# Optimization experiments

Hardware: AMD Instinct MI355X
Metric: run time of the kernel (lower is better)

Reference implementation:

```python
import jax, jax.numpy as jnp
import numpy as np

B, S, D, E, K = 4, 2048, 1024, 8, 2
H = 4 * D  # FFN hidden per expert


def setup_inputs() -> dict:
    key = jax.random.key(0)
    ks = jax.random.split(key, 5)
    s = 0.02  # init scale
    return {
        "x": jax.random.normal(ks[0], (B, S, D), dtype=jnp.float32),
        "Wg": jax.random.normal(ks[1], (D, E), dtype=jnp.float32) * s,
        "bg": jnp.zeros((E,), dtype=jnp.float32),
        "W1": jax.random.normal(ks[2], (E, D, H), dtype=jnp.float32) * s,
        "b1": jnp.zeros((E, H), dtype=jnp.float32),
        "W2": jax.random.normal(ks[3], (E, H, D), dtype=jnp.float32) * s,
        "b2": jnp.zeros((E, D), dtype=jnp.float32),
    }


def reference(x, Wg, bg, W1, b1, W2, b2):
    # Router: softmax over expert logits, then top-k (torch.topk semantics)
    probs = jax.nn.softmax(x @ Wg + bg, axis=-1)      # [B,S,E]
    w, idx = jax.lax.top_k(probs, K)                   # [B,S,K] each
    # Dense all-experts MLP (matches original: every expert runs on every token)
    h = jax.nn.gelu(jnp.einsum('bsd,edh->bseh', x, W1) + b1, approximate=False)  # [B,S,E,H]
    y = jnp.einsum('bseh,ehd->bsed', h, W2) + b2       # [B,S,E,D]
    # One-hot mask + weighted sum == gather selected experts, scale by w, sum over k
    yk = jnp.take_along_axis(y, idx[..., None], axis=2)  # [B,S,K,D]
    return jnp.sum(yk * w[..., None], axis=2)            # [B,S,D]
```

## Files before the change

kernel.cpp:

```cpp
#include <hip/hip_runtime.h>
#include <hip/hip_bf16.h>
#include <math.h>


#define TOK     8192
#define DMODEL  1024
#define NEXP    8
#define HFF     4096
#define NASSIGN 16384
#define SLOTPAD 16512
#define BM      128
#define BN      128
#define BK      64
#define MAXRT   135

typedef __attribute__((ext_vector_type(8))) short s16x8;
typedef __attribute__((ext_vector_type(4))) float f32x4;

__device__ __forceinline__ void gll16(const void* g, void* l) {
  __builtin_amdgcn_global_load_lds((const __attribute__((address_space(1))) void*)g,
                                   (__attribute__((address_space(3))) void*)l, 16, 0, 0);
}

__global__ void transpose_cvt(const float* __restrict__ in, __hip_bfloat16* __restrict__ out,
                              int R, int C) {
  __shared__ float t[64][65];
  const float* src = in + (size_t)blockIdx.z * R * C;
  __hip_bfloat16* dst = out + (size_t)blockIdx.z * R * C;
  const int r0 = blockIdx.y * 64, c0 = blockIdx.x * 64;
  const int tc = threadIdx.x & 63, tr = threadIdx.x >> 6;
#pragma unroll
  for (int i = 0; i < 16; ++i) {
    int r = i * 4 + tr;
    t[r][tc] = src[(size_t)(r0 + r) * C + c0 + tc];
  }
  __syncthreads();
  const int jl = (threadIdx.x & 15) * 4;
  const int cw = threadIdx.x >> 4;
#pragma unroll
  for (int p = 0; p < 4; ++p) {
    const int cc = p * 16 + cw;
    union { ushort4 u; __hip_bfloat16 h[4]; } o;
#pragma unroll
    for (int u = 0; u < 4; ++u) o.h[u] = __float2bfloat16(t[jl + u][cc]);
    *(ushort4*)(dst + (size_t)(c0 + cc) * R + r0 + jl) = o.u;
  }
}

__global__ void router_kernel(const float* __restrict__ x, const float* __restrict__ Wg,
                              const float* __restrict__ bg, int* __restrict__ idx,
                              float* __restrict__ wtok, int* __restrict__ counts) {
  __shared__ int scnt[NEXP];
  if (threadIdx.x < NEXP) scnt[threadIdx.x] = 0;
  __syncthreads();
  const int wave = threadIdx.x >> 6, lane = threadIdx.x & 63;
  const int t = blockIdx.x * 4 + wave;
  float acc[NEXP];
#pragma unroll
  for (int e = 0; e < NEXP; ++e) acc[e] = 0.f;
  const float* xr = x + (size_t)t * DMODEL + lane * 16;
#pragma unroll
  for (int j = 0; j < 4; ++j) {
    float4 xv = *(const float4*)(xr + j * 4);
    const float* wr = Wg + (size_t)(lane * 16 + j * 4) * NEXP;
#pragma unroll
    for (int u = 0; u < 4; ++u) {
      float xs = (&xv.x)[u];
      float4 w0 = *(const float4*)(wr + u * NEXP);
      float4 w1 = *(const float4*)(wr + u * NEXP + 4);
      acc[0] += xs * w0.x; acc[1] += xs * w0.y; acc[2] += xs * w0.z; acc[3] += xs * w0.w;
      acc[4] += xs * w1.x; acc[5] += xs * w1.y; acc[6] += xs * w1.z; acc[7] += xs * w1.w;
    }
  }
#pragma unroll
  for (int off = 32; off >= 1; off >>= 1) {
#pragma unroll
    for (int e = 0; e < NEXP; ++e) acc[e] += __shfl_xor(acc[e], off, 64);
  }
  if (lane == 0) {
    float l[NEXP], m = -1e30f;
#pragma unroll
    for (int e = 0; e < NEXP; ++e) { l[e] = acc[e] + bg[e]; m = fmaxf(m, l[e]); }
    float p[NEXP], s = 0.f;
#pragma unroll
    for (int e = 0; e < NEXP; ++e) { p[e] = expf(l[e] - m); s += p[e]; }
    float inv = 1.f / s;
#pragma unroll
    for (int e = 0; e < NEXP; ++e) p[e] *= inv;
    int i0 = 0; float v0 = p[0];
#pragma unroll
    for (int e = 1; e < NEXP; ++e) if (p[e] > v0) { v0 = p[e]; i0 = e; }
    int i1 = -1; float v1 = -1e30f;
#pragma unroll
    for (int e = 0; e < NEXP; ++e) if (e != i0 && p[e] > v1) { v1 = p[e]; i1 = e; }
    idx[2 * t] = i0; idx[2 * t + 1] = i1;
    wtok[2 * t] = v0; wtok[2 * t + 1] = v1;
    atomicAdd(&scnt[i0], 1); atomicAdd(&scnt[i1], 1);
  }
  __syncthreads();
  if (threadIdx.x < NEXP) atomicAdd(&counts[threadIdx.x], scnt[threadIdx.x]);
}

__global__ void scan_kernel(int* ctrl) {
  if (threadIdx.x == 0 && blockIdx.x == 0) {
    int* counts = ctrl;
    int* cursor = ctrl + 8;
    int* expOff = ctrl + 16;
    int* tro = ctrl + 26;
    expOff[0] = 0; tro[0] = 0;
    for (int e = 0; e < NEXP; ++e) {
      expOff[e + 1] = expOff[e] + counts[e];
      tro[e + 1] = tro[e] + (counts[e] + BM - 1) / BM;
      cursor[e] = expOff[e];
    }
  }
}

__global__ void scatter_kernel(const int* __restrict__ idx, const float* __restrict__ wtok,
                               int* ctrl, int* __restrict__ perm, float* __restrict__ wslot) {
  __shared__ int lcnt[NEXP];
  __shared__ int lbase[NEXP];
  const int t = blockIdx.x * 256 + threadIdx.x;
  if (threadIdx.x < NEXP) lcnt[threadIdx.x] = 0;
  __syncthreads();
  const int e0 = idx[2 * t], e1 = idx[2 * t + 1];
  const int l0 = atomicAdd(&lcnt[e0], 1);
  const int l1 = atomicAdd(&lcnt[e1], 1);
  __syncthreads();
  if (threadIdx.x < NEXP)
    lbase[threadIdx.x] = atomicAdd(&ctrl[8 + threadIdx.x], lcnt[threadIdx.x]);
  __syncthreads();
  const int s0 = lbase[e0] + l0, s1 = lbase[e1] + l1;
  perm[s0] = t; perm[s1] = t;
  wslot[s0] = wtok[2 * t]; wslot[s1] = wtok[2 * t + 1];
}

__global__ void gather_cvt_x(const float* __restrict__ x, const int* __restrict__ perm,
                             __hip_bfloat16* __restrict__ xg) {
  const int slot = blockIdx.x;
  const int t = perm[slot];
  const float4 v = *(const float4*)(x + (size_t)t * DMODEL + threadIdx.x * 4);
  union { ushort4 u; __hip_bfloat16 h[4]; } o;
  o.h[0] = __float2bfloat16(v.x); o.h[1] = __float2bfloat16(v.y);
  o.h[2] = __float2bfloat16(v.z); o.h[3] = __float2bfloat16(v.w);
  *(ushort4*)(xg + (size_t)slot * DMODEL + threadIdx.x * 4) = o.u;
}


__global__ __launch_bounds__(256, 3) void gemm1_kernel(
    const __hip_bfloat16* __restrict__ xg, const __hip_bfloat16* __restrict__ w1t,
    const float* __restrict__ b1, __hip_bfloat16* __restrict__ hbuf,
    const int* __restrict__ ctrl) {
  const int* expOff = ctrl + 16;
  const int* tro = ctrl + 26;
  const int w = blockIdx.x;
  const int rt = w >> 5, nt = w & 31;
  if (rt >= tro[NEXP]) return;
  int e = 0;
#pragma unroll
  for (int q = 1; q < NEXP; ++q) if (tro[q] <= rt) e = q;
  const int rowBase = expOff[e] + (rt - tro[e]) * BM;
  const int rowEnd = expOff[e + 1];

  __shared__ __hip_bfloat16 lA[BM * BK];
  __shared__ __hip_bfloat16 lB[BN * BK];

  const int tid = threadIdx.x;
  const int lane = tid & 63, wave = tid >> 6;
  const int quad = lane >> 4, lm = lane & 15;
  const int waveM = (wave >> 1) * 64, waveN = (wave & 1) * 64;

  f32x4 acc[4][4];
#pragma unroll
  for (int a = 0; a < 4; ++a)
#pragma unroll
    for (int b = 0; b < 4; ++b) acc[a][b] = (f32x4){0.f, 0.f, 0.f, 0.f};

  const __hip_bfloat16* bbase = w1t + (size_t)e * HFF * DMODEL + (size_t)nt * BN * DMODEL;
  const __hip_bfloat16* gA[4]; const __hip_bfloat16* gB[4];
  __hip_bfloat16* sA[4]; __hip_bfloat16* sB[4];
#pragma unroll
  for (int i = 0; i < 4; ++i) {
    const int s = tid + 256 * i;
    const int r = s >> 3, sl = s & 7, kc = sl ^ (r & 7);
    gA[i] = xg + (size_t)(rowBase + r) * DMODEL + kc * 8;
    gB[i] = bbase + (size_t)r * DMODEL + kc * 8;
    sA[i] = lA + s * 8; sB[i] = lB + s * 8;
  }

  int aOff[4], bOff[4];
#pragma unroll
  for (int tm = 0; tm < 4; ++tm) {
    int r = waveM + tm * 16 + lm;
    aOff[tm] = r * 64 + (quad ^ (r & 7)) * 8;
  }
#pragma unroll
  for (int tn = 0; tn < 4; ++tn) {
    int r = waveN + tn * 16 + lm;
    bOff[tn] = r * 64 + (quad ^ (r & 7)) * 8;
  }

  for (int kt = 0; kt < DMODEL / BK; ++kt) {
#pragma unroll
    for (int i = 0; i < 4; ++i) { gll16(gA[i], sA[i]); gll16(gB[i], sB[i]); }
#pragma unroll
    for (int i = 0; i < 4; ++i) { gA[i] += BK; gB[i] += BK; }
    __syncthreads();
#pragma unroll
    for (int h = 0; h < 2; ++h) {
      s16x8 af[4], bfr[4];
#pragma unroll
      for (int tm = 0; tm < 4; ++tm) af[tm] = *(const s16x8*)(lA + (aOff[tm] ^ (h * 32)));
#pragma unroll
      for (int tn = 0; tn < 4; ++tn) bfr[tn] = *(const s16x8*)(lB + (bOff[tn] ^ (h * 32)));
#pragma unroll
      for (int tm = 0; tm < 4; ++tm)
#pragma unroll
        for (int tn = 0; tn < 4; ++tn)
          acc[tm][tn] = __builtin_amdgcn_mfma_f32_16x16x32_bf16(af[tm], bfr[tn], acc[tm][tn], 0, 0, 0);
    }
    __syncthreads();
  }

  const int colBase = nt * BN + waveN;
  float bv[4];
#pragma unroll
  for (int tn = 0; tn < 4; ++tn) bv[tn] = b1[e * HFF + colBase + tn * 16 + lm];
#pragma unroll
  for (int tm = 0; tm < 4; ++tm) {
    const int rb = rowBase + waveM + tm * 16 + quad * 4;
#pragma unroll
    for (int reg = 0; reg < 4; ++reg) {
      const int row = rb + reg;
      if (row < rowEnd) {
#pragma unroll
        for (int tn = 0; tn < 4; ++tn) {
          float v = acc[tm][tn][reg] + bv[tn];
          v = 0.5f * v * (1.f + erff(v * 0.70710678118654752f));
          hbuf[(size_t)row * HFF + colBase + tn * 16 + lm] = __float2bfloat16(v);
        }
      }
    }
  }
}

__global__ __launch_bounds__(256, 3) void gemm2_kernel(
    const __hip_bfloat16* __restrict__ hbuf, const __hip_bfloat16* __restrict__ w2t,
    const float* __restrict__ b2, const float* __restrict__ wslot,
    const int* __restrict__ perm, float* __restrict__ out, const int* __restrict__ ctrl) {
  const int* expOff = ctrl + 16;
  const int* tro = ctrl + 26;
  const int w = blockIdx.x;
  const int rt = w >> 3, nt = w & 7;
  if (rt >= tro[NEXP]) return;
  int e = 0;
#pragma unroll
  for (int q = 1; q < NEXP; ++q) if (tro[q] <= rt) e = q;
  const int rowBase = expOff[e] + (rt - tro[e]) * BM;
  const int rowEnd = expOff[e + 1];

  __shared__ __hip_bfloat16 lA[BM * BK];
  __shared__ __hip_bfloat16 lB[BN * BK];

  const int tid = threadIdx.x;
  const int lane = tid & 63, wave = tid >> 6;
  const int quad = lane >> 4, lm = lane & 15;
  const int waveM = (wave >> 1) * 64, waveN = (wave & 1) * 64;

  f32x4 acc[4][4];
#pragma unroll
  for (int a = 0; a < 4; ++a)
#pragma unroll
    for (int b = 0; b < 4; ++b) acc[a][b] = (f32x4){0.f, 0.f, 0.f, 0.f};

  const __hip_bfloat16* bbase = w2t + (size_t)e * DMODEL * HFF + (size_t)nt * BN * HFF;
  const __hip_bfloat16* gA[4]; const __hip_bfloat16* gB[4];
  __hip_bfloat16* sA[4]; __hip_bfloat16* sB[4];
#pragma unroll
  for (int i = 0; i < 4; ++i) {
    const int s = tid + 256 * i;
    const int r = s >> 3, sl = s & 7, kc = sl ^ (r & 7);
    gA[i] = hbuf + (size_t)(rowBase + r) * HFF + kc * 8;
    gB[i] = bbase + (size_t)r * HFF + kc * 8;
    sA[i] = lA + s * 8; sB[i] = lB + s * 8;
  }

  int aOff[4], bOff[4];
#pragma unroll
  for (int tm = 0; tm < 4; ++tm) {
    int r = waveM + tm * 16 + lm;
    aOff[tm] = r * 64 + (quad ^ (r & 7)) * 8;
  }
#pragma unroll
  for (int tn = 0; tn < 4; ++tn) {
    int r = waveN + tn * 16 + lm;
    bOff[tn] = r * 64 + (quad ^ (r & 7)) * 8;
  }

  for (int kt = 0; kt < HFF / BK; ++kt) {
#pragma unroll
    for (int i = 0; i < 4; ++i) { gll16(gA[i], sA[i]); gll16(gB[i], sB[i]); }
#pragma unroll
    for (int i = 0; i < 4; ++i) { gA[i] += BK; gB[i] += BK; }
    __syncthreads();
#pragma unroll
    for (int h = 0; h < 2; ++h) {
      s16x8 af[4], bfr[4];
#pragma unroll
      for (int tm = 0; tm < 4; ++tm) af[tm] = *(const s16x8*)(lA + (aOff[tm] ^ (h * 32)));
#pragma unroll
      for (int tn = 0; tn < 4; ++tn) bfr[tn] = *(const s16x8*)(lB + (bOff[tn] ^ (h * 32)));
#pragma unroll
      for (int tm = 0; tm < 4; ++tm)
#pragma unroll
        for (int tn = 0; tn < 4; ++tn)
          acc[tm][tn] = __builtin_amdgcn_mfma_f32_16x16x32_bf16(af[tm], bfr[tn], acc[tm][tn], 0, 0, 0);
    }
    __syncthreads();
  }

  const int colBase = nt * BN + waveN;
  float bv[4];
#pragma unroll
  for (int tn = 0; tn < 4; ++tn) bv[tn] = b2[e * DMODEL + colBase + tn * 16 + lm];
#pragma unroll
  for (int tm = 0; tm < 4; ++tm) {
    const int rb = rowBase + waveM + tm * 16 + quad * 4;
#pragma unroll
    for (int reg = 0; reg < 4; ++reg) {
      const int row = rb + reg;
      if (row < rowEnd) {
        const float wr = wslot[row];
        float* orow = out + (size_t)perm[row] * DMODEL + colBase;
#pragma unroll
        for (int tn = 0; tn < 4; ++tn)
          atomicAdd(orow + tn * 16 + lm, (acc[tm][tn][reg] + bv[tn]) * wr);
      }
    }
  }
}

extern "C" void kernel_launch(void* const* d_in, const int* in_sizes, int n_in,
                              void* d_out, int out_size, void* d_ws, size_t ws_size,
                              hipStream_t stream) {
  const float* x  = (const float*)d_in[0];
  const float* Wg = (const float*)d_in[1];
  const float* bg = (const float*)d_in[2];
  const float* W1 = (const float*)d_in[3];
  const float* b1 = (const float*)d_in[4];
  const float* W2 = (const float*)d_in[5];
  const float* b2 = (const float*)d_in[6];
  float* out = (float*)d_out;

  char* ws = (char*)d_ws;
  size_t off = 0;
  auto take = [&](size_t bytes) -> char* {
    char* p = ws + off;
    off = (off + bytes + 255) & ~(size_t)255;
    return p;
  };
  int*   ctrl  = (int*)take(64 * sizeof(int));
  int*   idx   = (int*)take((size_t)TOK * 2 * 4);
  float* wtok  = (float*)take((size_t)TOK * 2 * 4);
  int*   perm  = (int*)take((size_t)SLOTPAD * 4);
  float* wslot = (float*)take((size_t)SLOTPAD * 4);
  __hip_bfloat16* W1t = (__hip_bfloat16*)take((size_t)NEXP * HFF * DMODEL * 2);
  __hip_bfloat16* W2t = (__hip_bfloat16*)take((size_t)NEXP * DMODEL * HFF * 2);
  __hip_bfloat16* xgb = (__hip_bfloat16*)take((size_t)SLOTPAD * DMODEL * 2);
  __hip_bfloat16* hb  = (__hip_bfloat16*)take((size_t)SLOTPAD * HFF * 2);
  (void)ws_size; (void)in_sizes; (void)n_in; (void)out_size;

  hipMemsetAsync(ctrl, 0, 64 * sizeof(int), stream);
  hipMemsetAsync(out, 0, (size_t)TOK * DMODEL * 4, stream);
  transpose_cvt<<<dim3(HFF / 64, DMODEL / 64, NEXP), 256, 0, stream>>>(W1, W1t, DMODEL, HFF);
  transpose_cvt<<<dim3(DMODEL / 64, HFF / 64, NEXP), 256, 0, stream>>>(W2, W2t, HFF, DMODEL);
  router_kernel<<<TOK / 4, 256, 0, stream>>>(x, Wg, bg, idx, wtok, ctrl);
  scan_kernel<<<1, 64, 0, stream>>>(ctrl);
  scatter_kernel<<<TOK / 256, 256, 0, stream>>>(idx, wtok, ctrl, perm, wslot);
  gather_cvt_x<<<NASSIGN, 256, 0, stream>>>(x, perm, xgb);
  gemm1_kernel<<<MAXRT * (HFF / BN), 256, 0, stream>>>(xgb, W1t, b1, hb, ctrl);
  gemm2_kernel<<<MAXRT * (DMODEL / BN), 256, 0, stream>>>(hb, W2t, b2, wslot, perm, out, ctrl);
}
```

Baseline: 794.5 us.

## Triple-buffer LDS tiles with async global-to-LDS prefetch in both expert GEMMs

Both grouped GEMMs move from a single-buffered load-sync-compute loop to a three-stage ring of LDS buffers. Tiles are prefetched two k-steps ahead with global_load_lds, and explicit vmcnt waits plus raw s_barrier calls replace __syncthreads. BK is halved to 32 and the LDS swizzle is changed to a rotation pattern, which keeps total LDS at 48KB per block. The aim is to hide global memory latency behind MFMA work. In exchange there are twice as many barrier iterations, and correctness depends on the hand-coded waitcnt encodings.

```diff
diff --git a/kernel.cpp b/kernel.cpp
--- a/kernel.cpp
+++ b/kernel.cpp
@@ -11,8 +11,9 @@
 #define SLOTPAD 16512
 #define BM      128
 #define BN      128
-#define BK      64
+#define BK      32
 #define MAXRT   135
+#define BUFSZ   8192
 
 typedef __attribute__((ext_vector_type(8))) short s16x8;
 typedef __attribute__((ext_vector_type(4))) float f32x4;
@@ -147,6 +148,10 @@
 }
 
 
+#define WAIT_VM8  __builtin_amdgcn_s_waitcnt(0xF78)
+#define WAIT_VM4  __builtin_amdgcn_s_waitcnt(0xF74)
+#define WAIT_VM0  __builtin_amdgcn_s_waitcnt(0xF70)
+
 __global__ __launch_bounds__(256, 3) void gemm1_kernel(
     const __hip_bfloat16* __restrict__ xg, const __hip_bfloat16* __restrict__ w1t,
     const float* __restrict__ b1, __hip_bfloat16* __restrict__ hbuf,
@@ -162,8 +167,7 @@
   const int rowBase = expOff[e] + (rt - tro[e]) * BM;
   const int rowEnd = expOff[e + 1];
 
-  __shared__ __hip_bfloat16 lA[BM * BK];
-  __shared__ __hip_bfloat16 lB[BN * BK];
+  __shared__ __hip_bfloat16 lds[3 * BUFSZ];
 
   const int tid = threadIdx.x;
   const int lane = tid & 63, wave = tid >> 6;
@@ -176,50 +180,57 @@
 #pragma unroll
     for (int b = 0; b < 4; ++b) acc[a][b] = (f32x4){0.f, 0.f, 0.f, 0.f};
 
+  const int c0 = tid, c1 = tid + 256;
+  const int r0 = c0 >> 2, r1 = c1 >> 2;
+  const int kc0 = ((c0 & 3) - ((r0 >> 1) & 3) + 4) & 3;
+  const int kc1 = ((c1 & 3) - ((r1 >> 1) & 3) + 4) & 3;
   const __hip_bfloat16* bbase = w1t + (size_t)e * HFF * DMODEL + (size_t)nt * BN * DMODEL;
-  const __hip_bfloat16* gA[4]; const __hip_bfloat16* gB[4];
-  __hip_bfloat16* sA[4]; __hip_bfloat16* sB[4];
-#pragma unroll
-  for (int i = 0; i < 4; ++i) {
-    const int s = tid + 256 * i;
-    const int r = s >> 3, sl = s & 7, kc = sl ^ (r & 7);
-    gA[i] = xg + (size_t)(rowBase + r) * DMODEL + kc * 8;
-    gB[i] = bbase + (size_t)r * DMODEL + kc * 8;
-    sA[i] = lA + s * 8; sB[i] = lB + s * 8;
-  }
+  const __hip_bfloat16* pA0 = xg + (size_t)(rowBase + r0) * DMODEL + kc0 * 8;
+  const __hip_bfloat16* pA1 = xg + (size_t)(rowBase + r1) * DMODEL + kc1 * 8;
+  const __hip_bfloat16* pB0 = bbase + (size_t)r0 * DMODEL + kc0 * 8;
+  const __hip_bfloat16* pB1 = bbase + (size_t)r1 * DMODEL + kc1 * 8;
+  const int lA0 = c0 * 8, lA1 = c1 * 8;
+
+#define ISSUE1(bi) { __hip_bfloat16* Lb = lds + (bi) * BUFSZ;                       \
+    gll16(pA0, Lb + lA0); gll16(pA1, Lb + lA1);                                     \
+    gll16(pB0, Lb + 4096 + lA0); gll16(pB1, Lb + 4096 + lA1);                       \
+    pA0 += BK; pA1 += BK; pB0 += BK; pB1 += BK; }
 
   int aOff[4], bOff[4];
 #pragma unroll
   for (int tm = 0; tm < 4; ++tm) {
     int r = waveM + tm * 16 + lm;
-    aOff[tm] = r * 64 + (quad ^ (r & 7)) * 8;
+    aOff[tm] = r * 32 + ((quad + (r >> 1)) & 3) * 8;
   }
 #pragma unroll
   for (int tn = 0; tn < 4; ++tn) {
     int r = waveN + tn * 16 + lm;
-    bOff[tn] = r * 64 + (quad ^ (r & 7)) * 8;
-  }
-
-  for (int kt = 0; kt < DMODEL / BK; ++kt) {
-#pragma unroll
-    for (int i = 0; i < 4; ++i) { gll16(gA[i], sA[i]); gll16(gB[i], sB[i]); }
-#pragma unroll
-    for (int i = 0; i < 4; ++i) { gA[i] += BK; gB[i] += BK; }
-    __syncthreads();
-#pragma unroll
-    for (int h = 0; h < 2; ++h) {
-      s16x8 af[4], bfr[4];
-#pragma unroll
-      for (int tm = 0; tm < 4; ++tm) af[tm] = *(const s16x8*)(lA + (aOff[tm] ^ (h * 32)));
-#pragma unroll
-      for (int tn = 0; tn < 4; ++tn) bfr[tn] = *(const s16x8*)(lB + (bOff[tn] ^ (h * 32)));
-#pragma unroll
-      for (int tm = 0; tm < 4; ++tm)
-#pragma unroll
-        for (int tn = 0; tn < 4; ++tn)
-          acc[tm][tn] = __builtin_amdgcn_mfma_f32_16x16x32_bf16(af[tm], bfr[tn], acc[tm][tn], 0, 0, 0);
-    }
-    __syncthreads();
+    bOff[tn] = 4096 + r * 32 + ((quad + (r >> 1)) & 3) * 8;
+  }
+
+  ISSUE1(0); ISSUE1(1);
+  int ib = 2, cb = 0;
+  const int NIT = DMODEL / BK;
+  for (int kt = 0; kt < NIT; ++kt) {
+    if (kt + 2 < NIT) { ISSUE1(ib); ib = (ib == 2) ? 0 : ib + 1; WAIT_VM8; }
+    else if (kt + 1 < NIT) { WAIT_VM4; }
+    else { WAIT_VM0; }
+    __builtin_amdgcn_s_barrier();
+    __builtin_amdgcn_sched_barrier(0);
+    const __hip_bfloat16* Lc = lds + cb * BUFSZ;
+    s16x8 af[4], bfr[4];
+#pragma unroll
+    for (int tm = 0; tm < 4; ++tm) af[tm] = *(const s16x8*)(Lc + aOff[tm]);
+#pragma unroll
+    for (int tn = 0; tn < 4; ++tn) bfr[tn] = *(const s16x8*)(Lc + bOff[tn]);
+#pragma unroll
+    for (int tm = 0; tm < 4; ++tm)
+#pragma unroll
+      for (int tn = 0; tn < 4; ++tn)
+        acc[tm][tn] = __builtin_amdgcn_mfma_f32_16x16x32_bf16(af[tm], bfr[tn], acc[tm][tn], 0, 0, 0);
+    cb = (cb == 2) ? 0 : cb + 1;
+    __builtin_amdgcn_sched_barrier(0);
+    __builtin_amdgcn_s_barrier();
   }
 
   const int colBase = nt * BN + waveN;
@@ -259,8 +270,7 @@
   const int rowBase = expOff[e] + (rt - tro[e]) * BM;
   const int rowEnd = expOff[e + 1];
 
-  __shared__ __hip_bfloat16 lA[BM * BK];
-  __shared__ __hip_bfloat16 lB[BN * BK];
+  __shared__ __hip_bfloat16 lds[3 * BUFSZ];
 
   const int tid = threadIdx.x;
   const int lane = tid & 63, wave = tid >> 6;
@@ -273,50 +283,57 @@
 #pragma unroll
     for (int b = 0; b < 4; ++b) acc[a][b] = (f32x4){0.f, 0.f, 0.f, 0.f};
 
+  const int c0 = tid, c1 = tid + 256;
+  const int r0 = c0 >> 2, r1 = c1 >> 2;
+  const int kc0 = ((c0 & 3) - ((r0 >> 1) & 3) + 4) & 3;
+  const int kc1 = ((c1 & 3) - ((r1 >> 1) & 3) + 4) & 3;
   const __hip_bfloat16* bbase = w2t + (size_t)e * DMODEL * HFF + (size_t)nt * BN * HFF;
-  const __hip_bfloat16* gA[4]; const __hip_bfloat16* gB[4];
-  __hip_bfloat16* sA[4]; __hip_bfloat16* sB[4];
-#pragma unroll
-  for (int i = 0; i < 4; ++i) {
-    const int s = tid + 256 * i;
-    const int r = s >> 3, sl = s & 7, kc = sl ^ (r & 7);
-    gA[i] = hbuf + (size_t)(rowBase + r) * HFF + kc * 8;
-    gB[i] = bbase + (size_t)r * HFF + kc * 8;
-    sA[i] = lA + s * 8; sB[i] = lB + s * 8;
-  }
+  const __hip_bfloat16* pA0 = hbuf + (size_t)(rowBase + r0) * HFF + kc0 * 8;
+  const __hip_bfloat16* pA1 = hbuf + (size_t)(rowBase + r1) * HFF + kc1 * 8;
+  const __hip_bfloat16* pB0 = bbase + (size_t)r0 * HFF + kc0 * 8;
+  const __hip_bfloat16* pB1 = bbase + (size_t)r1 * HFF + kc1 * 8;
+  const int lA0 = c0 * 8, lA1 = c1 * 8;
+
+#define ISSUE2(bi) { __hip_bfloat16* Lb = lds + (bi) * BUFSZ;                       \
+    gll16(pA0, Lb + lA0); gll16(pA1, Lb + lA1);                                     \
+    gll16(pB0, Lb + 4096 + lA0); gll16(pB1, Lb + 4096 + lA1);                       \
+    pA0 += BK; pA1 += BK; pB0 += BK; pB1 += BK; }
 
   int aOff[4], bOff[4];
 #pragma unroll
   for (int tm = 0; tm < 4; ++tm) {
     int r = waveM + tm * 16 + lm;
-    aOff[tm] = r * 64 + (quad ^ (r & 7)) * 8;
+    aOff[tm] = r * 32 + ((quad + (r >> 1)) & 3) * 8;
   }
 #pragma unroll
   for (int tn = 0; tn < 4; ++tn) {
     int r = waveN + tn * 16 + lm;
-    bOff[tn] = r * 64 + (quad ^ (r & 7)) * 8;
-  }
-
-  for (int kt = 0; kt < HFF / BK; ++kt) {
-#pragma unroll
-    for (int i = 0; i < 4; ++i) { gll16(gA[i], sA[i]); gll16(gB[i], sB[i]); }
-#pragma unroll
-    for (int i = 0; i < 4; ++i) { gA[i] += BK; gB[i] += BK; }
-    __syncthreads();
-#pragma unroll
-    for (int h = 0; h < 2; ++h) {
-      s16x8 af[4], bfr[4];
-#pragma unroll
-      for (int tm = 0; tm < 4; ++tm) af[tm] = *(const s16x8*)(lA + (aOff[tm] ^ (h * 32)));
-#pragma unroll
-      for (int tn = 0; tn < 4; ++tn) bfr[tn] = *(const s16x8*)(lB + (bOff[tn] ^ (h * 32)));
-#pragma unroll
-      for (int tm = 0; tm < 4; ++tm)
-#pragma unroll
-        for (int tn = 0; tn < 4; ++tn)
-          acc[tm][tn] = __builtin_amdgcn_mfma_f32_16x16x32_bf16(af[tm], bfr[tn], acc[tm][tn], 0, 0, 0);
-    }
-    __syncthreads();
+    bOff[tn] = 4096 + r * 32 + ((quad + (r >> 1)) & 3) * 8;
+  }
+
+  ISSUE2(0); ISSUE2(1);
+  int ib = 2, cb = 0;
+  const int NIT = HFF / BK;
+  for (int kt = 0; kt < NIT; ++kt) {
+    if (kt + 2 < NIT) { ISSUE2(ib); ib = (ib == 2) ? 0 : ib + 1; WAIT_VM8; }
+    else if (kt + 1 < NIT) { WAIT_VM4; }
+    else { WAIT_VM0; }
+    __builtin_amdgcn_s_barrier();
+    __builtin_amdgcn_sched_barrier(0);
+    const __hip_bfloat16* Lc = lds + cb * BUFSZ;
+    s16x8 af[4], bfr[4];
+#pragma unroll
+    for (int tm = 0; tm < 4; ++tm) af[tm] = *(const s16x8*)(Lc + aOff[tm]);
+#pragma unroll
+    for (int tn = 0; tn < 4; ++tn) bfr[tn] = *(const s16x8*)(Lc + bOff[tn]);
+#pragma unroll
+    for (int tm = 0; tm < 4; ++tm)
+#pragma unroll
+      for (int tn = 0; tn < 4; ++tn)
+        acc[tm][tn] = __builtin_amdgcn_mfma_f32_16x16x32_bf16(af[tm], bfr[tn], acc[tm][tn], 0, 0, 0);
+    cb = (cb == 2) ? 0 : cb + 1;
+    __builtin_amdgcn_sched_barrier(0);
+    __builtin_amdgcn_s_barrier();
   }
 
   const int colBase = nt * BN + waveN;
```

After: 806.6 us. Within noise of the previous version (+1.5%).
